# Kernel tuning notes

Measured on AMD Instinct MI355X. Metric: run time of the kernel, lower is better.

The kernel has to match this reference:

```python
import jax, jax.numpy as jnp
import numpy as np

NUM_ENTITY_TYPES = 32
B, Q, L = 64, 64, 4096


def hungarian(cost):
    """O(n^3) Hungarian algorithm (minimization) for a square cost matrix.
    Returns col_of_row: row i is assigned to column col_of_row[i].
    Matches scipy.optimize.linear_sum_assignment for square inputs
    (row indices ascending)."""
    n = cost.shape[0]
    INF = 1e18
    u = np.zeros(n + 1)
    v = np.zeros(n + 1)
    p = np.zeros(n + 1, dtype=np.int64)   # p[j] = row matched to col j (1-based, 0 = free)
    way = np.zeros(n + 1, dtype=np.int64)
    for i in range(1, n + 1):
        p[0] = i
        j0 = 0
        minv = np.full(n + 1, INF)
        used = np.zeros(n + 1, dtype=bool)
        while True:
            used[j0] = True
            i0 = p[j0]
            cur = cost[i0 - 1, :] - u[i0] - v[1:]
            upd = (~used[1:]) & (cur < minv[1:])
            minv[1:][upd] = cur[upd]
            way[1:][upd] = j0
            free = ~used[1:]
            j1 = 1 + int(np.argmin(np.where(free, minv[1:], INF)))
            delta = minv[j1]
            u[p[used]] += delta
            v[used] -= delta
            minv[~used] -= delta
            j0 = j1
            if p[j0] == 0:
                break
        while j0:
            j1 = way[j0]
            p[j0] = p[j1]
            j0 = j1
    col_of_row = np.zeros(n, dtype=np.int64)
    for j in range(1, n + 1):
        col_of_row[p[j] - 1] = j - 1
    return col_of_row


def _match(start_pred, end_pred, tag_pred, start_label, end_label, tag_label):
    """Vectorized cost construction (the fused-kernel candidate), then per-sample
    Hungarian solve on CPU (inherently sequential, as in the original)."""
    # span coordinates from argmax of position logits  [B,Q,2]
    sp = jnp.stack([jnp.argmax(start_pred, -1), jnp.argmax(end_pred, -1)], -1).astype(jnp.float32)
    sl = jnp.stack([start_label, end_label], -1).astype(jnp.float32)
    # L1 cdist: [B,Qp,Ql]
    span_cost = jnp.sum(jnp.abs(sp[:, :, None, :] - sl[:, None, :, :]), -1)
    p_left, p_right = sp.min(-1), sp.max(-1)   # [B,Qp]
    l_left, l_right = sl.min(-1), sl.max(-1)   # [B,Ql]
    i_left = jnp.maximum(p_left[:, :, None], l_left[:, None, :])
    # NOTE: faithful to the original's bug: intersect_right = min(span_p_right, span_p_right)
    i_right = jnp.broadcast_to(p_right[:, :, None], i_left.shape)
    intersect = jnp.maximum(i_right - i_left, 0.0)
    u_left = jnp.minimum(p_left[:, :, None], l_left[:, None, :])
    u_right = jnp.maximum(p_right[:, :, None], l_right[:, None, :])
    union = jnp.maximum(u_right - u_left, 1e-10)
    iou_cost = -intersect / union
    # class cost: -softmax(tag_p)[:, tag_l]  -> [B,Qp,Ql]
    tag_sm = jax.nn.softmax(tag_pred, -1)                       # [B,Q,E]
    idx = jnp.broadcast_to(tag_label[:, None, :], (tag_sm.shape[0], tag_sm.shape[1], tag_label.shape[1]))
    class_cost = -jnp.take_along_axis(tag_sm, idx, axis=2)
    cost = np.asarray(span_cost + iou_cost + class_cost, dtype=np.float64)
    # masks are all-true by construction (tag_pred has exactly E classes,
    # tag_label < E), so shapes are static and cost is square.
    j_perm = np.stack([hungarian(cost[b]) for b in range(cost.shape[0])])  # [B,Q]
    return jnp.asarray(j_perm)


def _ce_per_sample(logits, targets):
    # logits [B,Q,C], targets [B,Q] -> mean CE over Q per sample: [B]
    logp = jax.nn.log_softmax(logits, -1)
    nll = -jnp.take_along_axis(logp, targets[..., None], axis=-1)[..., 0]
    return jnp.mean(nll, axis=-1)


def reference(start_pred, end_pred, tag_pred, start_label, end_label, tag_label):
    j = _match(start_pred, end_pred, tag_pred, start_label, end_label, tag_label)  # [B,Q]
    # row indices i == arange(Q) (square matcher), so preds stay in order and
    # labels are permuted by j.
    tgt_s = jnp.take_along_axis(start_label, j, axis=1)
    tgt_e = jnp.take_along_axis(end_label, j, axis=1)
    tgt_t = jnp.take_along_axis(tag_label, j, axis=1)
    per_sample = (_ce_per_sample(start_pred, tgt_s)
                  + _ce_per_sample(end_pred, tgt_e)
                  + _ce_per_sample(tag_pred, tgt_t))
    loss = jnp.mean(per_sample)
    return loss, j


def setup_inputs() -> dict:
    key = jax.random.key(0)
    k1, k2, k3, k4, k5, k6 = jax.random.split(key, 6)
    return {
        "start_pred": jax.random.normal(k1, (B, Q, L), dtype=jnp.float32),
        "end_pred": jax.random.normal(k2, (B, Q, L), dtype=jnp.float32),
        "tag_pred": jax.random.normal(k3, (B, Q, NUM_ENTITY_TYPES), dtype=jnp.float32),
        "start_label": jax.random.randint(k4, (B, Q), 0, L, dtype=jnp.int64) if jax.config.read('jax_enable_x64') else jax.random.randint(k4, (B, Q), 0, L).astype(jnp.int64),
        "end_label": jax.random.randint(k5, (B, Q), 0, L).astype(jnp.int64),
        "tag_label": jax.random.randint(k6, (B, Q), 0, NUM_ENTITY_TYPES).astype(jnp.int64),
    }


if __name__ == "__main__":
    out = reference(**setup_inputs())
    print(out[0], out[1].shape)
```

## Files before the change

kernel.cpp:

```cpp
#include <hip/hip_runtime.h>
#include <math.h>

#define BB 64
#define QQ 64
#define LLEN 4096
#define NE 32

__global__ __launch_bounds__(256) void rowstat_kernel(
    const float* __restrict__ sp, const float* __restrict__ ep,
    int* __restrict__ amax, float* __restrict__ lse)
{
    int rid = blockIdx.x;
    const float* base = (rid < BB * QQ) ? (sp + (size_t)rid * LLEN)
                                        : (ep + (size_t)(rid - BB * QQ) * LLEN);
    int t = threadIdx.x;
    const float4* b4 = (const float4*)base;
    float4 v[4];
#pragma unroll
    for (int k = 0; k < 4; k++) v[k] = b4[t + k * 256];

    float bm = -INFINITY; int bi = 0x7fffffff;
#pragma unroll
    for (int k = 0; k < 4; k++) {
        float a[4] = { v[k].x, v[k].y, v[k].z, v[k].w };
        int base_i = (t + k * 256) * 4;
#pragma unroll
        for (int c = 0; c < 4; c++) {
            int idx = base_i + c;
            if (a[c] > bm || (a[c] == bm && idx < bi)) { bm = a[c]; bi = idx; }
        }
    }
#pragma unroll
    for (int off = 32; off >= 1; off >>= 1) {
        float om = __shfl_xor(bm, off);
        int   oi = __shfl_xor(bi, off);
        if (om > bm || (om == bm && oi < bi)) { bm = om; bi = oi; }
    }
    __shared__ float smax[4]; __shared__ int sidx[4];
    int wave = t >> 6, lane = t & 63;
    if (lane == 0) { smax[wave] = bm; sidx[wave] = bi; }
    __syncthreads();
    float fm = smax[0]; int fi = sidx[0];
#pragma unroll
    for (int w = 1; w < 4; w++) {
        float om = smax[w]; int oi = sidx[w];
        if (om > fm || (om == fm && oi < fi)) { fm = om; fi = oi; }
    }

    float s = 0.f;
#pragma unroll
    for (int k = 0; k < 4; k++) {
        float a[4] = { v[k].x, v[k].y, v[k].z, v[k].w };
#pragma unroll
        for (int c = 0; c < 4; c++) s += __expf(a[c] - fm);
    }
#pragma unroll
    for (int off = 32; off >= 1; off >>= 1) s += __shfl_xor(s, off);
    __shared__ float ssum[4];
    if (lane == 0) ssum[wave] = s;
    __syncthreads();
    if (t == 0) {
        float tot = ssum[0] + ssum[1] + ssum[2] + ssum[3];
        amax[rid] = fi;
        lse[rid]  = fm + logf(tot);
    }
}

__device__ __forceinline__ double readlane_f64(double x, int l) {
    union { double d; int i[2]; } u; u.d = x;
    int lo = __builtin_amdgcn_readlane(u.i[0], l);
    int hi = __builtin_amdgcn_readlane(u.i[1], l);
    union { int i[2]; double d; } r; r.i[0] = lo; r.i[1] = hi;
    return r.d;
}

__device__ __forceinline__ unsigned int wave_min_u32(unsigned int x) {
    int xi = (int)x;
#define DPP_MIN_STEP(ctrl)                                                     \
    {                                                                          \
        int yi = __builtin_amdgcn_update_dpp(-1, xi, ctrl, 0xf, 0xf, false);   \
        unsigned int a = (unsigned int)xi, bq = (unsigned int)yi;              \
        xi = (int)(a < bq ? a : bq);                                           \
    }
    DPP_MIN_STEP(0x111)
    DPP_MIN_STEP(0x112)
    DPP_MIN_STEP(0x114)
    DPP_MIN_STEP(0x118)
    DPP_MIN_STEP(0x142)
    DPP_MIN_STEP(0x143)
#undef DPP_MIN_STEP
    return (unsigned int)__builtin_amdgcn_readlane(xi, 63);
}

__global__ __launch_bounds__(64) void match_kernel(
    const float* __restrict__ start_pred, const float* __restrict__ end_pred,
    const float* __restrict__ tag_pred,
    const int* __restrict__ s_label, const int* __restrict__ e_label,
    const int* __restrict__ t_label,
    const int* __restrict__ amax_all, const float* __restrict__ lse_all,
    float* __restrict__ out, double* __restrict__ persample)
{
    int b = blockIdx.x;
    int lane = threadIdx.x;

    __shared__ float cost[QQ * QQ];
    __shared__ float tagrow[QQ * NE];
    __shared__ int   sl_s[QQ], sl_e[QQ], sl_t[QQ];
    __shared__ float sps[QQ], spe[QQ];
    __shared__ float qmax[QQ], qden[QQ];
    __shared__ int   colOfRow[QQ];

    const float4* tp4 = (const float4*)(tag_pred + (size_t)b * QQ * NE);
    float4* tr4 = (float4*)tagrow;
    for (int k = lane; k < 512; k += 64) tr4[k] = tp4[k];
    sl_s[lane] = s_label[b * QQ + lane];
    sl_e[lane] = e_label[b * QQ + lane];
    sl_t[lane] = t_label[b * QQ + lane];
    sps[lane] = (float)amax_all[b * QQ + lane];
    spe[lane] = (float)amax_all[BB * QQ + b * QQ + lane];
    __syncthreads();

    {
        float mx = tagrow[lane * NE];
        for (int c = 1; c < NE; c++) mx = fmaxf(mx, tagrow[lane * NE + c]);
        float den = 0.f;
        for (int c = 0; c < NE; c++) {
            float d = tagrow[lane * NE + c] - mx;
            float u = (float)exp((double)d);
            den += u;
        }
        qmax[lane] = mx; qden[lane] = den;
    }
    __syncthreads();

    {
        float ls = (float)sl_s[lane], le = (float)sl_e[lane];
        float l_l = fminf(ls, le), l_r = fmaxf(ls, le);
        int   tl = sl_t[lane];
        for (int qp = 0; qp < QQ; qp++) {
            float ps = sps[qp], pe = spe[qp];
            float span = fabsf(ps - ls) + fabsf(pe - le);
            float p_l = fminf(ps, pe), p_r = fmaxf(ps, pe);
            float i_l = fmaxf(p_l, l_l);
            float inter = fmaxf(p_r - i_l, 0.f);
            float u_l2 = fminf(p_l, l_l), u_r = fmaxf(p_r, l_r);
            float uni = fmaxf(u_r - u_l2, 1e-10f);
            float iou = (-inter) / uni;
            float x = tagrow[qp * NE + tl];
            float unn = (float)exp((double)(x - qmax[qp]));
            float cls = -(unn / qden[qp]);
            cost[qp * QQ + lane] = (span + iou) + cls;
        }
    }
    __syncthreads();

    const double INFV = 1e18;
    const unsigned long long infb = __builtin_bit_cast(unsigned long long, 1e18);
    const unsigned int INFHI_T = (unsigned int)(infb >> 32) | 0x80000000u;

    double v_l = 0.0;
    double u_l = 0.0;
    int    p_l = 0;

    for (int i = 1; i <= QQ; i++) {
        int p0 = i;
        int j0 = 0;
        double minv_l = INFV;
        int    way_l = 0;
        bool   used_l = false;
        bool   rowUsed_l = false;
        int r = i - 1;
        float  cpre = cost[r * QQ + lane];
        double upre = readlane_f64(u_l, r);
        double delta = 0.0;
        for (;;) {
            if (j0 != 0 && lane == j0 - 1) used_l = true;
            if (lane == r) rowUsed_l = true;
            if (!used_l) minv_l -= delta;
            double cur = ((double)cpre - upre) - v_l;
            if (!used_l && cur < minv_l) { minv_l = cur; way_l = j0; }

            unsigned long long kb = __builtin_bit_cast(unsigned long long, minv_l);
            unsigned int kbhi = (unsigned int)(kb >> 32);
            unsigned int kblo = (unsigned int)kb;
            bool neg = (int)kbhi < 0;
            unsigned int tihi = neg ? ~kbhi : (kbhi | 0x80000000u);
            unsigned int tilo = neg ? ~kblo : kblo;
            unsigned int keyhi = used_l ? INFHI_T : tihi;
            unsigned int mhi = wave_min_u32(keyhi);
            bool hieq = (keyhi == mhi);
            unsigned int lo2 = hieq ? tilo : 0xFFFFFFFFu;
            unsigned int mlo = wave_min_u32(lo2);
            unsigned long long mask = __ballot(hieq && (lo2 == mlo));
            int l = __ffsll((long long)mask) - 1;
            int j1 = l + 1;
            unsigned long long kmin = ((unsigned long long)mhi << 32) | mlo;
            unsigned long long db = (kmin & 0x8000000000000000ull)
                                    ? (kmin ^ 0x8000000000000000ull) : ~kmin;
            delta = __builtin_bit_cast(double, db);

            int pj1 = __builtin_amdgcn_readlane(p_l, l);
            int rc = (pj1 - 1) & 63;
            float  cnext = cost[rc * QQ + lane];
            double unext = readlane_f64(u_l, rc);

            if (rowUsed_l) u_l += delta;
            if (used_l)   v_l -= delta;
            j0 = j1;
            if (pj1 == 0) break;
            r = rc; cpre = cnext; upre = unext;
        }
        while (j0 != 0) {
            int j1a = __builtin_amdgcn_readlane(way_l, j0 - 1);
            int pj1 = (j1a == 0) ? p0 : __builtin_amdgcn_readlane(p_l, j1a - 1);
            if (lane == j0 - 1) p_l = pj1;
            j0 = j1a;
        }
    }

    colOfRow[p_l - 1] = lane;
    __syncthreads();
    int jq = colOfRow[lane];
    out[1 + b * QQ + lane] = (float)jq;

    int ts = sl_s[jq], te = sl_e[jq], tt = sl_t[jq];
    float lses = lse_all[b * QQ + lane];
    float lsee = lse_all[BB * QQ + b * QQ + lane];
    float xs = start_pred[((size_t)(b * QQ + lane)) * LLEN + ts];
    float xe = end_pred[((size_t)(b * QQ + lane)) * LLEN + te];
    float xt = tagrow[lane * NE + tt];
    double ce = ((double)lses - (double)xs)
              + ((double)lsee - (double)xe)
              + ((double)qmax[lane] + log((double)qden[lane]) - (double)xt);
#pragma unroll
    for (int off = 32; off >= 1; off >>= 1) ce += __shfl_xor(ce, off);
    if (lane == 0) persample[b] = ce / 64.0;
}

__global__ __launch_bounds__(64) void final_kernel(
    const double* __restrict__ persample, float* __restrict__ out)
{
    int lane = threadIdx.x;
    double v = persample[lane];
#pragma unroll
    for (int off = 32; off >= 1; off >>= 1) v += __shfl_xor(v, off);
    if (lane == 0) out[0] = (float)(v / 64.0);
}

extern "C" void kernel_launch(void* const* d_in, const int* in_sizes, int n_in,
                              void* d_out, int out_size, void* d_ws, size_t ws_size,
                              hipStream_t stream)
{
    const float* start_pred = (const float*)d_in[0];
    const float* end_pred   = (const float*)d_in[1];
    const float* tag_pred   = (const float*)d_in[2];
    const int*   s_label    = (const int*)d_in[3];
    const int*   e_label    = (const int*)d_in[4];
    const int*   t_label    = (const int*)d_in[5];
    float* out = (float*)d_out;

    int*    amax = (int*)d_ws;
    float*  lse  = (float*)((char*)d_ws + 8192 * sizeof(int));
    double* ps   = (double*)((char*)d_ws + 8192 * sizeof(int) + 8192 * sizeof(float));

    rowstat_kernel<<<2 * BB * QQ, 256, 0, stream>>>(start_pred, end_pred, amax, lse);
    match_kernel<<<BB, QQ, 0, stream>>>(start_pred, end_pred, tag_pred,
                                        s_label, e_label, t_label,
                                        amax, lse, out, ps);
    final_kernel<<<1, QQ, 0, stream>>>(ps, out);
}
```

Measured before the change: 313.0 us.

## Keep Hungarian cost matrix in registers and shortcut the argmin reduction

Each lane now holds its 64-entry cost column in two 32-wide register vectors instead of shared memory. The serial Hungarian loop reads the next row's cost with a wave-uniform index rather than an LDS load, and the shared-memory barrier after building the costs is gone. The argmin now runs the second wave-min over the low word only when more than one lane ties on the high word, and the sign-flip key transforms use branchless XOR. The trade-off is more VGPRs per lane, and the compiler may lower the dynamic vector indexing to a select chain or scratch memory.

```diff
diff --git a/kernel.cpp b/kernel.cpp
--- a/kernel.cpp
+++ b/kernel.cpp
@@ -5,6 +5,8 @@
 #define QQ 64
 #define LLEN 4096
 #define NE 32
+
+typedef float f32x32 __attribute__((ext_vector_type(32)));
 
 __global__ __launch_bounds__(256) void rowstat_kernel(
     const float* __restrict__ sp, const float* __restrict__ ep,
@@ -103,7 +105,6 @@
     int b = blockIdx.x;
     int lane = threadIdx.x;
 
-    __shared__ float cost[QQ * QQ];
     __shared__ float tagrow[QQ * NE];
     __shared__ int   sl_s[QQ], sl_e[QQ], sl_t[QQ];
     __shared__ float sps[QQ], spe[QQ];
@@ -133,26 +134,32 @@
     }
     __syncthreads();
 
+    f32x32 cA, cB;
     {
         float ls = (float)sl_s[lane], le = (float)sl_e[lane];
         float l_l = fminf(ls, le), l_r = fmaxf(ls, le);
         int   tl = sl_t[lane];
-        for (int qp = 0; qp < QQ; qp++) {
-            float ps = sps[qp], pe = spe[qp];
-            float span = fabsf(ps - ls) + fabsf(pe - le);
-            float p_l = fminf(ps, pe), p_r = fmaxf(ps, pe);
-            float i_l = fmaxf(p_l, l_l);
-            float inter = fmaxf(p_r - i_l, 0.f);
-            float u_l2 = fminf(p_l, l_l), u_r = fmaxf(p_r, l_r);
-            float uni = fmaxf(u_r - u_l2, 1e-10f);
-            float iou = (-inter) / uni;
-            float x = tagrow[qp * NE + tl];
-            float unn = (float)exp((double)(x - qmax[qp]));
-            float cls = -(unn / qden[qp]);
-            cost[qp * QQ + lane] = (span + iou) + cls;
-        }
-    }
-    __syncthreads();
+#define COST_ROW(qp, DST, SLOT)                                               \
+        {                                                                     \
+            float ps = sps[qp], pe = spe[qp];                                 \
+            float span = fabsf(ps - ls) + fabsf(pe - le);                     \
+            float p_l = fminf(ps, pe), p_r = fmaxf(ps, pe);                   \
+            float i_l = fmaxf(p_l, l_l);                                      \
+            float inter = fmaxf(p_r - i_l, 0.f);     \
+            float u_l2 = fminf(p_l, l_l), u_r = fmaxf(p_r, l_r);              \
+            float uni = fmaxf(u_r - u_l2, 1e-10f);                            \
+            float iou = (-inter) / uni;                  \
+            float x = tagrow[(qp) * NE + tl];                                 \
+            float unn = (float)exp((double)(x - qmax[qp]));                   \
+            float cls = -(unn / qden[qp]);                                    \
+            DST[SLOT] = (span + iou) + cls;                                   \
+        }
+#pragma unroll
+        for (int qp = 0; qp < 32; qp++) COST_ROW(qp, cA, qp)
+#pragma unroll
+        for (int qp = 32; qp < 64; qp++) COST_ROW(qp, cB, qp - 32)
+#undef COST_ROW
+    }
 
     const double INFV = 1e18;
     const unsigned long long infb = __builtin_bit_cast(unsigned long long, 1e18);
@@ -170,45 +177,51 @@
         bool   used_l = false;
         bool   rowUsed_l = false;
         int r = i - 1;
-        float  cpre = cost[r * QQ + lane];
-        double upre = readlane_f64(u_l, r);
+        double cur = ((double)((r & 32) ? cB[r & 31] : cA[r & 31])
+                      - readlane_f64(u_l, r)) - v_l;
         double delta = 0.0;
         for (;;) {
             if (j0 != 0 && lane == j0 - 1) used_l = true;
             if (lane == r) rowUsed_l = true;
             if (!used_l) minv_l -= delta;
-            double cur = ((double)cpre - upre) - v_l;
             if (!used_l && cur < minv_l) { minv_l = cur; way_l = j0; }
 
             unsigned long long kb = __builtin_bit_cast(unsigned long long, minv_l);
             unsigned int kbhi = (unsigned int)(kb >> 32);
             unsigned int kblo = (unsigned int)kb;
-            bool neg = (int)kbhi < 0;
-            unsigned int tihi = neg ? ~kbhi : (kbhi | 0x80000000u);
-            unsigned int tilo = neg ? ~kblo : kblo;
+            unsigned int sm = (unsigned int)((int)kbhi >> 31);
+            unsigned int tihi = kbhi ^ (sm | 0x80000000u);
+            unsigned int tilo = kblo ^ sm;
             unsigned int keyhi = used_l ? INFHI_T : tihi;
             unsigned int mhi = wave_min_u32(keyhi);
             bool hieq = (keyhi == mhi);
-            unsigned int lo2 = hieq ? tilo : 0xFFFFFFFFu;
-            unsigned int mlo = wave_min_u32(lo2);
-            unsigned long long mask = __ballot(hieq && (lo2 == mlo));
-            int l = __ffsll((long long)mask) - 1;
-            int j1 = l + 1;
-            unsigned long long kmin = ((unsigned long long)mhi << 32) | mlo;
-            unsigned long long db = (kmin & 0x8000000000000000ull)
-                                    ? (kmin ^ 0x8000000000000000ull) : ~kmin;
-            delta = __builtin_bit_cast(double, db);
+            unsigned long long hmask = __ballot(hieq);
+            int l; unsigned int mlo;
+            if (__popcll(hmask) == 1) {
+                l = __ffsll((long long)hmask) - 1;
+                mlo = (unsigned int)__builtin_amdgcn_readlane((int)tilo, l);
+            } else {
+                unsigned int lo2 = hieq ? tilo : 0xFFFFFFFFu;
+                mlo = wave_min_u32(lo2);
+                unsigned long long mask = __ballot(hieq && (lo2 == mlo));
+                l = __ffsll((long long)mask) - 1;
+            }
+            unsigned int dsm = ~(unsigned int)((int)mhi >> 31);
+            unsigned int dhi = mhi ^ (dsm | 0x80000000u);
+            unsigned int dlo = mlo ^ dsm;
+            delta = __builtin_bit_cast(double,
+                        ((unsigned long long)dhi << 32) | dlo);
 
             int pj1 = __builtin_amdgcn_readlane(p_l, l);
             int rc = (pj1 - 1) & 63;
-            float  cnext = cost[rc * QQ + lane];
-            double unext = readlane_f64(u_l, rc);
+            double cn = ((double)((rc & 32) ? cB[rc & 31] : cA[rc & 31])
+                         - readlane_f64(u_l, rc)) - v_l;
 
             if (rowUsed_l) u_l += delta;
             if (used_l)   v_l -= delta;
-            j0 = j1;
+            j0 = l + 1;
             if (pj1 == 0) break;
-            r = rc; cpre = cnext; upre = unext;
+            r = rc; cur = cn;
         }
         while (j0 != 0) {
             int j1a = __builtin_amdgcn_readlane(way_l, j0 - 1);
```

Result: slower. 326.3 us (+4.2%).
